# Optimization experiments

Hardware: AMD Instinct MI355X
Metric: run time of the kernel (lower is better)

The kernel has to match this reference:

```python
import jax, jax.numpy as jnp
import numpy as np

N_NODES = 100000
N_EDGES = 1600000
IN_C, HID_C, OUT_C = 128, 128, 64


def setup_inputs() -> dict:
    key = jax.random.key(0)
    k1, k2, k3, k4 = jax.random.split(key, 4)
    x = jax.random.normal(k1, (N_NODES, IN_C), dtype=jnp.float32)
    edge_index = jax.random.randint(k2, (2, N_EDGES), 0, N_NODES, dtype=jnp.int32)
    # Glorot-ish init for linear weights, zero bias (PyG GCNConv default bias=0)
    W1 = jax.random.normal(k3, (IN_C, HID_C), dtype=jnp.float32) / np.sqrt(IN_C)
    b1 = jnp.zeros((HID_C,), dtype=jnp.float32)
    W2 = jax.random.normal(k4, (HID_C, OUT_C), dtype=jnp.float32) / np.sqrt(HID_C)
    b2 = jnp.zeros((OUT_C,), dtype=jnp.float32)
    return {"x": x, "edge_index": edge_index, "W1": W1, "b1": b1, "W2": W2, "b2": b2}


def gcn_conv(x, edge_index, W, b, n_nodes):
    """PyG GCNConv: out = D^{-1/2} (A + I) D^{-1/2} (x W) + b."""
    h = x @ W  # [N, C_out]
    loop = jnp.arange(n_nodes, dtype=edge_index.dtype)
    src = jnp.concatenate([edge_index[0], loop])  # messages flow src -> dst
    dst = jnp.concatenate([edge_index[1], loop])
    # degree at destination nodes (includes self-loops)
    deg = jax.ops.segment_sum(jnp.ones_like(src, dtype=h.dtype), dst,
                              num_segments=n_nodes)
    dis = jnp.where(deg > 0, jax.lax.rsqrt(jnp.maximum(deg, 1e-12)), 0.0)
    norm = dis[src] * dis[dst]  # [E+N]
    msg = h[src] * norm[:, None]  # gather + scale
    out = jax.ops.segment_sum(msg, dst, num_segments=n_nodes)  # scatter-add
    return out + b


def reference(x, edge_index, W1, b1, W2, b2):
    h = jax.nn.relu(gcn_conv(x, edge_index, W1, b1, N_NODES))
    return gcn_conv(h, edge_index, W2, b2, N_NODES)
```

## Files before the change

### kernel.cpp

```cpp
#include <hip/hip_runtime.h>

#define N_NODES 100000
#define N_EDGES 1600000
#define IN_C 128
#define HID_C 128
#define OUT_C 64

#define SH 8
#define NBKT 391
#define CAP 4608
#define EPB 2048
#define EPT 8

typedef __attribute__((ext_vector_type(8))) short bf16x8;
typedef __attribute__((ext_vector_type(4))) float f32x4;

static __device__ __forceinline__ unsigned f2bf(float f) {
  union { float f; unsigned u; } v; v.f = f;
  unsigned r = v.u + 0x7fffu + ((v.u >> 16) & 1u);
  return r >> 16;
}
static __device__ __forceinline__ float bf2f(unsigned hu) {
  union { unsigned u; float f; } v; v.u = hu << 16; return v.f;
}
static __device__ __forceinline__ float bflo(unsigned u) {
  union { unsigned u; float f; } v; v.u = u << 16; return v.f;
}
static __device__ __forceinline__ float bfhi(unsigned u) {
  union { unsigned u; float f; } v; v.u = u & 0xffff0000u; return v.f;
}


__global__ __launch_bounds__(256) void k_partA(const int* __restrict__ src,
                                               const int* __restrict__ dst,
                                               int* __restrict__ bcnt,
                                               unsigned* __restrict__ tmp, int e) {
  __shared__ unsigned stage[EPB];
  __shared__ unsigned short bid[EPB];
  __shared__ int hist[NBKT];
  __shared__ int lstart[NBKT];
  __shared__ int base[NBKT];
  __shared__ int ps[256];
  const int t = threadIdx.x;
  const int e0 = blockIdx.x * EPB;
  const int m = (e0 + EPB < e ? EPB : e - e0);

  for (int i = t; i < NBKT; i += 256) hist[i] = 0;
  __syncthreads();

  int rsrc[EPT], rdst[EPT];
#pragma unroll
  for (int i = 0; i < EPT; ++i) {
    int idx = e0 + i * 256 + t;
    if (idx < e) {
      rsrc[i] = src[idx];
      rdst[i] = dst[idx];
      atomicAdd(&hist[rdst[i] >> SH], 1);
    }
  }
  __syncthreads();

  int a0 = (2 * t < NBKT) ? hist[2 * t] : 0;
  int a1 = (2 * t + 1 < NBKT) ? hist[2 * t + 1] : 0;
  ps[t] = a0 + a1;
  __syncthreads();
  for (int off = 1; off < 256; off <<= 1) {
    int add = (t >= off) ? ps[t - off] : 0;
    __syncthreads();
    ps[t] += add;
    __syncthreads();
  }
  int ex = ps[t] - (a0 + a1);
  if (2 * t < NBKT) lstart[2 * t] = ex;
  if (2 * t + 1 < NBKT) lstart[2 * t + 1] = ex + a0;

  for (int i = t; i < NBKT; i += 256) {
    int h = hist[i];
    base[i] = h ? atomicAdd(&bcnt[i], h) : 0;
    hist[i] = 0;
  }
  __syncthreads();

#pragma unroll
  for (int i = 0; i < EPT; ++i) {
    int idx = e0 + i * 256 + t;
    if (idx < e) {
      int d = rdst[i];
      int b = d >> SH;
      int pos = lstart[b] + atomicAdd(&hist[b], 1);
      stage[pos] = (unsigned)rsrc[i] | ((unsigned)(d & 255) << 17);
      bid[pos] = (unsigned short)b;
    }
  }
  __syncthreads();

  for (int pos = t; pos < m; pos += 256) {
    int b = bid[pos];
    int slot = base[b] + (pos - lstart[b]);
    if (slot < CAP)
      tmp[(size_t)b * CAP + slot] = stage[pos];
  }
}

__global__ __launch_bounds__(512) void k_bscan(const int* __restrict__ bcnt,
                                               int* __restrict__ bstart) {
  __shared__ int s[512];
  const int t = threadIdx.x;
  int v = 0;
  if (t < NBKT) {
    v = bcnt[t];
    if (v > CAP) v = CAP;
  }
  s[t] = v;
  __syncthreads();
  for (int off = 1; off < 512; off <<= 1) {
    int add = (t >= off) ? s[t - off] : 0;
    __syncthreads();
    s[t] += add;
    __syncthreads();
  }
  if (t <= NBKT) bstart[t] = s[t] - v;
}

__global__ __launch_bounds__(256) void k_bucket(const unsigned* __restrict__ tmp,
                                                const int* __restrict__ bcnt,
                                                const int* __restrict__ bstart,
                                                int* __restrict__ rowptr,
                                                int* __restrict__ col,
                                                float* __restrict__ dis, int n) {
  __shared__ int h[256];
  __shared__ int s[256];
  const int b = blockIdx.x, t = threadIdx.x;
  h[t] = 0;
  __syncthreads();
  int m = bcnt[b];
  if (m > CAP) m = CAP;
  const unsigned* tb = tmp + (size_t)b * CAP;
  for (int j = t; j < m; j += 256)
    atomicAdd(&h[tb[j] >> 17], 1);
  __syncthreads();
  const int node = (b << SH) + t;
  const int v = h[t];
  if (node < n) dis[node] = rsqrtf((float)(v + 1));
  s[t] = v;
  __syncthreads();
  for (int off = 1; off < 256; off <<= 1) {
    int add = (t >= off) ? s[t - off] : 0;
    __syncthreads();
    s[t] += add;
    __syncthreads();
  }
  const int base = bstart[b];
  const int ex = s[t] - v;
  if (node < n) rowptr[node] = base + ex;
  if (b == 0 && t == 0) rowptr[n] = bstart[NBKT];
  __syncthreads();
  h[t] = base + ex;
  __syncthreads();
  for (int j = t; j < m; j += 256) {
    unsigned u = tb[j];
    int pos = atomicAdd(&h[u >> 17], 1);
    col[pos] = (int)(u & 0x1FFFFu);
  }
}


__global__ void k_prepW(const float* __restrict__ W1, const float* __restrict__ W2,
                        unsigned short* __restrict__ W1h, unsigned short* __restrict__ W1l,
                        unsigned short* __restrict__ W2h, unsigned short* __restrict__ W2l) {
  int i = blockIdx.x * blockDim.x + threadIdx.x;
  if (i < IN_C * HID_C) {
    int k = i >> 7, c = i & 127;
    float w = W1[i];
    unsigned hi = f2bf(w);
    W1h[c * 128 + k] = (unsigned short)hi;
    W1l[c * 128 + k] = (unsigned short)f2bf(w - bf2f(hi));
  }
  int j = i - IN_C * HID_C;
  if (j >= 0 && j < HID_C * OUT_C) {
    int k = j >> 6, c = j & 63;
    float w = W2[j];
    unsigned hi = f2bf(w);
    W2h[c * 128 + k] = (unsigned short)hi;
    W2l[c * 128 + k] = (unsigned short)f2bf(w - bf2f(hi));
  }
}


__global__ __launch_bounds__(256) void k_mfma1(const float* __restrict__ X,
                                               const unsigned short* __restrict__ Wh,
                                               const unsigned short* __restrict__ Wl,
                                               const float* __restrict__ dis,
                                               unsigned short* __restrict__ Hs, int n) {
  __shared__ unsigned short xs[64 * 136];
  const int t = threadIdx.x;
  const int w = t >> 6, l = t & 63;
  const int lr = l & 15, lk = (l >> 4) * 8;
  const int row0 = blockIdx.x * 64;

  bf16x8 Bh[2][4], Bl[2][4];
#pragma unroll
  for (int c2 = 0; c2 < 2; ++c2)
#pragma unroll
    for (int kb = 0; kb < 4; ++kb) {
      int colw = w * 32 + c2 * 16 + lr;
      Bh[c2][kb] = *(const bf16x8*)&Wh[(size_t)colw * 128 + kb * 32 + lk];
      Bl[c2][kb] = *(const bf16x8*)&Wl[(size_t)colw * 128 + kb * 32 + lk];
    }

  for (int i = t; i < 64 * 32; i += 256) {
    int r = i >> 5, q = i & 31;
    float4 v = make_float4(0.f, 0.f, 0.f, 0.f);
    if (row0 + r < n) v = ((const float4*)(X + (size_t)(row0 + r) * IN_C))[q];
    unsigned p0 = f2bf(v.x) | (f2bf(v.y) << 16);
    unsigned p1 = f2bf(v.z) | (f2bf(v.w) << 16);
    *(uint2*)&xs[r * 136 + q * 4] = make_uint2(p0, p1);
  }
  __syncthreads();

#pragma unroll
  for (int rst = 0; rst < 4; ++rst) {
    bf16x8 a[4];
#pragma unroll
    for (int kb = 0; kb < 4; ++kb)
      a[kb] = *(const bf16x8*)&xs[(rst * 16 + lr) * 136 + kb * 32 + lk];
    f32x4 acc0 = (f32x4){0.f, 0.f, 0.f, 0.f};
    f32x4 acc1 = (f32x4){0.f, 0.f, 0.f, 0.f};
#pragma unroll
    for (int kb = 0; kb < 4; ++kb) {
      acc0 = __builtin_amdgcn_mfma_f32_16x16x32_bf16(a[kb], Bh[0][kb], acc0, 0, 0, 0);
      acc1 = __builtin_amdgcn_mfma_f32_16x16x32_bf16(a[kb], Bh[1][kb], acc1, 0, 0, 0);
      acc0 = __builtin_amdgcn_mfma_f32_16x16x32_bf16(a[kb], Bl[0][kb], acc0, 0, 0, 0);
      acc1 = __builtin_amdgcn_mfma_f32_16x16x32_bf16(a[kb], Bl[1][kb], acc1, 0, 0, 0);
    }
    const int rbase = row0 + rst * 16 + (l >> 4) * 4;
    float dv[4];
#pragma unroll
    for (int j = 0; j < 4; ++j) dv[j] = (rbase + j < n) ? dis[rbase + j] : 0.f;
#pragma unroll
    for (int c2 = 0; c2 < 2; ++c2) {
      int colw = w * 32 + c2 * 16 + lr;
      const f32x4& acc = c2 ? acc1 : acc0;
#pragma unroll
      for (int j = 0; j < 4; ++j) {
        int row = rbase + j;
        if (row < n) Hs[(size_t)row * HID_C + colw] = (unsigned short)f2bf(acc[j] * dv[j]);
      }
    }
  }
}


__global__ __launch_bounds__(256) void k_mfma2(const unsigned* __restrict__ G,
                                               const unsigned short* __restrict__ Wh,
                                               const unsigned short* __restrict__ Wl,
                                               const float* __restrict__ dis,
                                               unsigned short* __restrict__ Hs, int n) {
  __shared__ unsigned short xs[64 * 136];
  const int t = threadIdx.x;
  const int w = t >> 6, l = t & 63;
  const int lr = l & 15, lk = (l >> 4) * 8;
  const int row0 = blockIdx.x * 64;

  bf16x8 Bh[4], Bl[4];
#pragma unroll
  for (int kb = 0; kb < 4; ++kb) {
    int colw = w * 16 + lr;
    Bh[kb] = *(const bf16x8*)&Wh[(size_t)colw * 128 + kb * 32 + lk];
    Bl[kb] = *(const bf16x8*)&Wl[(size_t)colw * 128 + kb * 32 + lk];
  }

  for (int i = t; i < 64 * 32; i += 256) {
    int r = i >> 5, q = i & 31;
    uint2 v = make_uint2(0u, 0u);
    if (row0 + r < n) v = *(const uint2*)&G[(size_t)(row0 + r) * 64 + q * 2];
    *(uint2*)&xs[r * 136 + q * 4] = v;
  }
  __syncthreads();

#pragma unroll
  for (int rst = 0; rst < 4; ++rst) {
    bf16x8 a[4];
#pragma unroll
    for (int kb = 0; kb < 4; ++kb)
      a[kb] = *(const bf16x8*)&xs[(rst * 16 + lr) * 136 + kb * 32 + lk];
    f32x4 acc = (f32x4){0.f, 0.f, 0.f, 0.f};
#pragma unroll
    for (int kb = 0; kb < 4; ++kb) {
      acc = __builtin_amdgcn_mfma_f32_16x16x32_bf16(a[kb], Bh[kb], acc, 0, 0, 0);
      acc = __builtin_amdgcn_mfma_f32_16x16x32_bf16(a[kb], Bl[kb], acc, 0, 0, 0);
    }
    const int rbase = row0 + rst * 16 + (l >> 4) * 4;
    const int colw = w * 16 + lr;
#pragma unroll
    for (int j = 0; j < 4; ++j) {
      int row = rbase + j;
      if (row < n) Hs[(size_t)row * OUT_C + colw] =
          (unsigned short)f2bf(acc[j] * dis[row]);
    }
  }
}


__global__ __launch_bounds__(256) void k_agg128(const unsigned* __restrict__ Hs,
                                                const int* __restrict__ rowptr,
                                                const int* __restrict__ col,
                                                const float* __restrict__ dis,
                                                const float* __restrict__ bias,
                                                unsigned* __restrict__ G, int n) {
  const int node = (blockIdx.x * blockDim.x + threadIdx.x) >> 6;
  const int lane = threadIdx.x & 63;
  if (node >= n) return;
  unsigned u = Hs[(size_t)node * 64 + lane];
  float a0 = bflo(u), a1 = bfhi(u);
  int j = rowptr[node];
  const int end = rowptr[node + 1];
  for (; j + 8 <= end; j += 8) {
    int s0 = col[j], s1 = col[j + 1], s2 = col[j + 2], s3 = col[j + 3];
    int s4 = col[j + 4], s5 = col[j + 5], s6 = col[j + 6], s7 = col[j + 7];
    unsigned u0 = Hs[(size_t)s0 * 64 + lane];
    unsigned u1 = Hs[(size_t)s1 * 64 + lane];
    unsigned u2 = Hs[(size_t)s2 * 64 + lane];
    unsigned u3 = Hs[(size_t)s3 * 64 + lane];
    unsigned u4 = Hs[(size_t)s4 * 64 + lane];
    unsigned u5 = Hs[(size_t)s5 * 64 + lane];
    unsigned u6 = Hs[(size_t)s6 * 64 + lane];
    unsigned u7 = Hs[(size_t)s7 * 64 + lane];
    a0 += ((bflo(u0) + bflo(u1)) + (bflo(u2) + bflo(u3))) +
          ((bflo(u4) + bflo(u5)) + (bflo(u6) + bflo(u7)));
    a1 += ((bfhi(u0) + bfhi(u1)) + (bfhi(u2) + bfhi(u3))) +
          ((bfhi(u4) + bfhi(u5)) + (bfhi(u6) + bfhi(u7)));
  }
  for (; j + 4 <= end; j += 4) {
    int s0 = col[j], s1 = col[j + 1], s2 = col[j + 2], s3 = col[j + 3];
    unsigned u0 = Hs[(size_t)s0 * 64 + lane];
    unsigned u1 = Hs[(size_t)s1 * 64 + lane];
    unsigned u2 = Hs[(size_t)s2 * 64 + lane];
    unsigned u3 = Hs[(size_t)s3 * 64 + lane];
    a0 += (bflo(u0) + bflo(u1)) + (bflo(u2) + bflo(u3));
    a1 += (bfhi(u0) + bfhi(u1)) + (bfhi(u2) + bfhi(u3));
  }
  for (; j < end; ++j) {
    unsigned uu = Hs[(size_t)col[j] * 64 + lane];
    a0 += bflo(uu);
    a1 += bfhi(uu);
  }
  const float di = dis[node];
  const int c = lane * 2;
  float r0 = fmaxf(fmaf(a0, di, bias[c]), 0.f);
  float r1 = fmaxf(fmaf(a1, di, bias[c + 1]), 0.f);
  G[(size_t)node * 64 + lane] = f2bf(r0) | (f2bf(r1) << 16);
}

__global__ __launch_bounds__(256) void k_agg64(const unsigned* __restrict__ Hs,
                                               const int* __restrict__ rowptr,
                                               const int* __restrict__ col,
                                               const float* __restrict__ dis,
                                               const float* __restrict__ bias,
                                               float* __restrict__ out, int n) {
  const int node = (blockIdx.x * blockDim.x + threadIdx.x) >> 5;
  const int l = threadIdx.x & 31;
  if (node >= n) return;
  unsigned u = Hs[(size_t)node * 32 + l];
  float a0 = bflo(u), a1 = bfhi(u);
  int j = rowptr[node];
  const int end = rowptr[node + 1];
  for (; j + 8 <= end; j += 8) {
    int s0 = col[j], s1 = col[j + 1], s2 = col[j + 2], s3 = col[j + 3];
    int s4 = col[j + 4], s5 = col[j + 5], s6 = col[j + 6], s7 = col[j + 7];
    unsigned u0 = Hs[(size_t)s0 * 32 + l];
    unsigned u1 = Hs[(size_t)s1 * 32 + l];
    unsigned u2 = Hs[(size_t)s2 * 32 + l];
    unsigned u3 = Hs[(size_t)s3 * 32 + l];
    unsigned u4 = Hs[(size_t)s4 * 32 + l];
    unsigned u5 = Hs[(size_t)s5 * 32 + l];
    unsigned u6 = Hs[(size_t)s6 * 32 + l];
    unsigned u7 = Hs[(size_t)s7 * 32 + l];
    a0 += ((bflo(u0) + bflo(u1)) + (bflo(u2) + bflo(u3))) +
          ((bflo(u4) + bflo(u5)) + (bflo(u6) + bflo(u7)));
    a1 += ((bfhi(u0) + bfhi(u1)) + (bfhi(u2) + bfhi(u3))) +
          ((bfhi(u4) + bfhi(u5)) + (bfhi(u6) + bfhi(u7)));
  }
  for (; j + 4 <= end; j += 4) {
    int s0 = col[j], s1 = col[j + 1], s2 = col[j + 2], s3 = col[j + 3];
    unsigned u0 = Hs[(size_t)s0 * 32 + l];
    unsigned u1 = Hs[(size_t)s1 * 32 + l];
    unsigned u2 = Hs[(size_t)s2 * 32 + l];
    unsigned u3 = Hs[(size_t)s3 * 32 + l];
    a0 += (bflo(u0) + bflo(u1)) + (bflo(u2) + bflo(u3));
    a1 += (bfhi(u0) + bfhi(u1)) + (bfhi(u2) + bfhi(u3));
  }
  for (; j < end; ++j) {
    unsigned uu = Hs[(size_t)col[j] * 32 + l];
    a0 += bflo(uu);
    a1 += bfhi(uu);
  }
  const float di = dis[node];
  const int c = l * 2;
  float r0 = fmaf(a0, di, bias[c]);
  float r1 = fmaf(a1, di, bias[c + 1]);
  *(float2*)&out[(size_t)node * 64 + c] = make_float2(r0, r1);
}


extern "C" void kernel_launch(void* const* d_in, const int* in_sizes, int n_in,
                              void* d_out, int out_size, void* d_ws, size_t ws_size,
                              hipStream_t stream) {
  const float* x  = (const float*)d_in[0];
  const int*   ei = (const int*)d_in[1];
  const float* W1 = (const float*)d_in[2];
  const float* b1 = (const float*)d_in[3];
  const float* W2 = (const float*)d_in[4];
  const float* b2 = (const float*)d_in[5];
  float* out = (float*)d_out;

  const int N = N_NODES, E = N_EDGES;
  const int* esrc = ei;
  const int* edst = ei + E;

  char* w = (char*)d_ws;
  auto alloc = [&](size_t bytes) -> char* {
    char* p = w;
    w += (bytes + 255) & ~(size_t)255;
    return p;
  };
  float* dis          = (float*)alloc((size_t)N * 4);
  int* rowptr         = (int*)alloc((size_t)(N + 1) * 4);
  int* bcnt           = (int*)alloc((size_t)NBKT * 4);
  int* bstart         = (int*)alloc((size_t)(NBKT + 1) * 4);
  int* col            = (int*)alloc((size_t)E * 4);
  unsigned* tmp       = (unsigned*)alloc((size_t)NBKT * CAP * 4);
  unsigned short* h1s = (unsigned short*)alloc((size_t)N * HID_C * 2);
  unsigned* g1        = (unsigned*)alloc((size_t)N * (HID_C / 2) * 4);
  unsigned short* h2s = (unsigned short*)alloc((size_t)N * OUT_C * 2);
  unsigned short* W1h = (unsigned short*)alloc((size_t)IN_C * HID_C * 2);
  unsigned short* W1l = (unsigned short*)alloc((size_t)IN_C * HID_C * 2);
  unsigned short* W2h = (unsigned short*)alloc((size_t)HID_C * OUT_C * 2);
  unsigned short* W2l = (unsigned short*)alloc((size_t)HID_C * OUT_C * 2);

  hipMemsetAsync(bcnt, 0, (size_t)NBKT * 4, stream);
  k_partA<<<(E + EPB - 1) / EPB, 256, 0, stream>>>(esrc, edst, bcnt, tmp, E);
  k_bscan<<<1, 512, 0, stream>>>(bcnt, bstart);
  k_bucket<<<NBKT, 256, 0, stream>>>(tmp, bcnt, bstart, rowptr, col, dis, N);
  k_prepW<<<(IN_C * HID_C + HID_C * OUT_C + 255) / 256, 256, 0, stream>>>(
      W1, W2, W1h, W1l, W2h, W2l);

  k_mfma1<<<(N + 63) / 64, 256, 0, stream>>>(x, W1h, W1l, dis, h1s, N);
  k_agg128<<<(N * 64 + 255) / 256, 256, 0, stream>>>((const unsigned*)h1s, rowptr, col,
                                                     dis, b1, g1, N);
  k_mfma2<<<(N + 63) / 64, 256, 0, stream>>>(g1, W2h, W2l, dis, h2s, N);
  k_agg64<<<(N * 32 + 255) / 256, 256, 0, stream>>>((const unsigned*)h2s, rowptr, col,
                                                    dis, b2, out, N);
}
```

Measured before the change: 209.9 us.

## Split hidden features into two 64-column planes for layer-1 aggregation

The first GEMM now writes its bf16 output as two separate 64-column planes (column-split layout) instead of one 128-wide row. The layer-1 aggregation then runs half-width: each 32-lane group gathers 128-byte rows from one plane, and adjacent blocks alternate between planes. The intent is to shrink the gather working set per pass so the L2/MALL cache hits more often during random neighbour reads. The cost is twice as many col/rowptr reads and a wider, more scattered GEMM store pattern.

```diff
diff --git a/kernel.cpp b/kernel.cpp
--- a/kernel.cpp
+++ b/kernel.cpp
@@ -191,7 +191,7 @@
                                                const unsigned short* __restrict__ Wh,
                                                const unsigned short* __restrict__ Wl,
                                                const float* __restrict__ dis,
-                                               unsigned short* __restrict__ Hs, int n) {
+                                               unsigned short* __restrict__ Hb, int n) {
   __shared__ unsigned short xs[64 * 136];
   const int t = threadIdx.x;
   const int w = t >> 6, l = t & 63;
@@ -240,11 +240,14 @@
 #pragma unroll
     for (int c2 = 0; c2 < 2; ++c2) {
       int colw = w * 32 + c2 * 16 + lr;
+      const int grp = colw >> 6;
+      const int within = colw & 63;
       const f32x4& acc = c2 ? acc1 : acc0;
 #pragma unroll
       for (int j = 0; j < 4; ++j) {
         int row = rbase + j;
-        if (row < n) Hs[(size_t)row * HID_C + colw] = (unsigned short)f2bf(acc[j] * dv[j]);
+        if (row < n)
+          Hb[((size_t)grp * n + row) * 64 + within] = (unsigned short)f2bf(acc[j] * dv[j]);
       }
     }
   }
@@ -302,30 +305,33 @@
 }
 
 
-__global__ __launch_bounds__(256) void k_agg128(const unsigned* __restrict__ Hs,
-                                                const int* __restrict__ rowptr,
-                                                const int* __restrict__ col,
-                                                const float* __restrict__ dis,
-                                                const float* __restrict__ bias,
-                                                unsigned* __restrict__ G, int n) {
-  const int node = (blockIdx.x * blockDim.x + threadIdx.x) >> 6;
-  const int lane = threadIdx.x & 63;
+__global__ __launch_bounds__(256) void k_agg128s(const unsigned* __restrict__ Hb,
+                                                 const int* __restrict__ rowptr,
+                                                 const int* __restrict__ col,
+                                                 const float* __restrict__ dis,
+                                                 const float* __restrict__ bias,
+                                                 unsigned* __restrict__ G, int n) {
+  const int bid = blockIdx.x;
+  const int g = bid & 1;
+  const int node = (bid >> 1) * 8 + (threadIdx.x >> 5);
+  const int l = threadIdx.x & 31;
   if (node >= n) return;
-  unsigned u = Hs[(size_t)node * 64 + lane];
+  const unsigned* T = Hb + (size_t)g * n * 32;
+  unsigned u = T[(size_t)node * 32 + l];
   float a0 = bflo(u), a1 = bfhi(u);
   int j = rowptr[node];
   const int end = rowptr[node + 1];
   for (; j + 8 <= end; j += 8) {
     int s0 = col[j], s1 = col[j + 1], s2 = col[j + 2], s3 = col[j + 3];
     int s4 = col[j + 4], s5 = col[j + 5], s6 = col[j + 6], s7 = col[j + 7];
-    unsigned u0 = Hs[(size_t)s0 * 64 + lane];
-    unsigned u1 = Hs[(size_t)s1 * 64 + lane];
-    unsigned u2 = Hs[(size_t)s2 * 64 + lane];
-    unsigned u3 = Hs[(size_t)s3 * 64 + lane];
-    unsigned u4 = Hs[(size_t)s4 * 64 + lane];
-    unsigned u5 = Hs[(size_t)s5 * 64 + lane];
-    unsigned u6 = Hs[(size_t)s6 * 64 + lane];
-    unsigned u7 = Hs[(size_t)s7 * 64 + lane];
+    unsigned u0 = T[(size_t)s0 * 32 + l];
+    unsigned u1 = T[(size_t)s1 * 32 + l];
+    unsigned u2 = T[(size_t)s2 * 32 + l];
+    unsigned u3 = T[(size_t)s3 * 32 + l];
+    unsigned u4 = T[(size_t)s4 * 32 + l];
+    unsigned u5 = T[(size_t)s5 * 32 + l];
+    unsigned u6 = T[(size_t)s6 * 32 + l];
+    unsigned u7 = T[(size_t)s7 * 32 + l];
     a0 += ((bflo(u0) + bflo(u1)) + (bflo(u2) + bflo(u3))) +
           ((bflo(u4) + bflo(u5)) + (bflo(u6) + bflo(u7)));
     a1 += ((bfhi(u0) + bfhi(u1)) + (bfhi(u2) + bfhi(u3))) +
@@ -333,24 +339,25 @@
   }
   for (; j + 4 <= end; j += 4) {
     int s0 = col[j], s1 = col[j + 1], s2 = col[j + 2], s3 = col[j + 3];
-    unsigned u0 = Hs[(size_t)s0 * 64 + lane];
-    unsigned u1 = Hs[(size_t)s1 * 64 + lane];
-    unsigned u2 = Hs[(size_t)s2 * 64 + lane];
-    unsigned u3 = Hs[(size_t)s3 * 64 + lane];
+    unsigned u0 = T[(size_t)s0 * 32 + l];
+    unsigned u1 = T[(size_t)s1 * 32 + l];
+    unsigned u2 = T[(size_t)s2 * 32 + l];
+    unsigned u3 = T[(size_t)s3 * 32 + l];
     a0 += (bflo(u0) + bflo(u1)) + (bflo(u2) + bflo(u3));
     a1 += (bfhi(u0) + bfhi(u1)) + (bfhi(u2) + bfhi(u3));
   }
   for (; j < end; ++j) {
-    unsigned uu = Hs[(size_t)col[j] * 64 + lane];
+    unsigned uu = T[(size_t)col[j] * 32 + l];
     a0 += bflo(uu);
     a1 += bfhi(uu);
   }
   const float di = dis[node];
-  const int c = lane * 2;
+  const int c = g * 64 + l * 2;
   float r0 = fmaxf(fmaf(a0, di, bias[c]), 0.f);
   float r1 = fmaxf(fmaf(a1, di, bias[c + 1]), 0.f);
-  G[(size_t)node * 64 + lane] = f2bf(r0) | (f2bf(r1) << 16);
-}
+  G[(size_t)node * 64 + g * 32 + l] = f2bf(r0) | (f2bf(r1) << 16);
+}
+
 
 __global__ __launch_bounds__(256) void k_agg64(const unsigned* __restrict__ Hs,
                                                const int* __restrict__ rowptr,
@@ -430,7 +437,7 @@
   int* bstart         = (int*)alloc((size_t)(NBKT + 1) * 4);
   int* col            = (int*)alloc((size_t)E * 4);
   unsigned* tmp       = (unsigned*)alloc((size_t)NBKT * CAP * 4);
-  unsigned short* h1s = (unsigned short*)alloc((size_t)N * HID_C * 2);
+  unsigned short* h1b = (unsigned short*)alloc((size_t)2 * N * 64 * 2);
   unsigned* g1        = (unsigned*)alloc((size_t)N * (HID_C / 2) * 4);
   unsigned short* h2s = (unsigned short*)alloc((size_t)N * OUT_C * 2);
   unsigned short* W1h = (unsigned short*)alloc((size_t)IN_C * HID_C * 2);
@@ -445,9 +452,9 @@
   k_prepW<<<(IN_C * HID_C + HID_C * OUT_C + 255) / 256, 256, 0, stream>>>(
       W1, W2, W1h, W1l, W2h, W2l);
 
-  k_mfma1<<<(N + 63) / 64, 256, 0, stream>>>(x, W1h, W1l, dis, h1s, N);
-  k_agg128<<<(N * 64 + 255) / 256, 256, 0, stream>>>((const unsigned*)h1s, rowptr, col,
-                                                     dis, b1, g1, N);
+  k_mfma1<<<(N + 63) / 64, 256, 0, stream>>>(x, W1h, W1l, dis, h1b, N);
+  k_agg128s<<<((N + 7) / 8) * 2, 256, 0, stream>>>((const unsigned*)h1b, rowptr, col,
+                                                   dis, b1, g1, N);
   k_mfma2<<<(N + 63) / 64, 256, 0, stream>>>(g1, W2h, W2l, dis, h2s, N);
   k_agg64<<<(N * 32 + 255) / 256, 256, 0, stream>>>((const unsigned*)h2s, rowptr, col,
                                                     dis, b2, out, N);
```

After: 213.8 us. No clear change (+1.9%).
